# Performance work log

Hardware: AMD Instinct MI355X
Metric: run time of the kernel (lower is better)

## Reference

```python
import jax, jax.numpy as jnp
import numpy as np

B, N, FEAT, HID = 1024, 128, 512, 256


def setup_inputs() -> dict:
    key = jax.random.key(0)
    k1, k2, k3, k4, k5, k6 = jax.random.split(key, 6)
    x = jax.random.normal(k1, (B, FEAT), dtype=jnp.float32)
    labels = jax.random.randint(k2, (B,), 0, N, dtype=jnp.int64)
    W_proj = jax.random.normal(k3, (FEAT, HID), dtype=jnp.float32) / np.sqrt(FEAT)
    b_proj = jax.random.normal(k4, (HID,), dtype=jnp.float32) * 0.01
    means = jax.random.normal(k5, (N, HID), dtype=jnp.float32)
    # inverse covariances must be SPD so sqrt(dist_sq) is real
    A = jax.random.normal(k6, (N, HID, HID), dtype=jnp.float32)
    inv_covs = jnp.einsum('nij,nkj->nik', A, A) / HID + 0.1 * jnp.eye(HID, dtype=jnp.float32)
    return {"x": x, "labels": labels, "W_proj": W_proj, "b_proj": b_proj,
            "means": means, "inv_covs": inv_covs}


def reference(x, labels, W_proj, b_proj, means, inv_covs):
    b = x.shape[0]
    n = means.shape[0]
    x_proj = x @ W_proj + b_proj                       # (b, hid)
    delta = x_proj[:, None, :] - means[None, :, :]     # (b, n, hid)
    # batched Mahalanobis quadratic form
    dist_sq = jnp.einsum('bni,nij,bnj->bn', delta, inv_covs, delta)
    distmat = jnp.sqrt(dist_sq + 1e-12)                # (b, n)
    center_mask = (labels[:, None] == jnp.arange(n)[None, :]).astype(distmat.dtype)
    loss = jnp.clip(distmat * center_mask, 1e-12, 1e12).sum() / b
    return loss, distmat
```

## Files before the change

### kernel.cpp

```cpp
#include <hip/hip_runtime.h>
#include <hip/hip_bf16.h>

#define B_    1024
#define N_    128
#define FEAT_ 512
#define HID_  256

typedef __bf16 bf16x8 __attribute__((ext_vector_type(8)));
typedef float  f32x4  __attribute__((ext_vector_type(4)));

__device__ __forceinline__ unsigned int f2bf(float f) {
    unsigned int u = __float_as_uint(f);
    u += 0x7fffu + ((u >> 16) & 1u);
    return u >> 16;
}
__device__ __forceinline__ unsigned int pack2(float a, float b) {
    return f2bf(a) | (f2bf(b) << 16);
}

__global__ __launch_bounds__(256) void prep_kernel(
    const float* __restrict__ x, const float* __restrict__ W,
    const float* __restrict__ bias, const float* __restrict__ means,
    const float* __restrict__ invcov,
    float* __restrict__ xp, unsigned short* __restrict__ xbf,
    unsigned short* __restrict__ Mbf, float* __restrict__ v2,
    float* __restrict__ cpart)
{
    const int t = threadIdx.x;
    if (blockIdx.x < 512) {
        __shared__ float sv[64][33];
        const int n  = blockIdx.x >> 2;
        const int jq = blockIdx.x & 3;
        const float* Mn = invcov + (size_t)n * (HID_ * HID_) + (size_t)jq * 64 * HID_;
        const float* mu = means + (size_t)n * HID_;
        unsigned short* Mb = Mbf + (size_t)n * (HID_ * HID_) + (size_t)jq * 64 * HID_;
        const int gc = t & 31;
        const int r0 = t >> 5;
        const float4 mk0 = *(const float4*)(mu + gc * 8);
        const float4 mk1 = *(const float4*)(mu + gc * 8 + 4);
        #pragma unroll
        for (int i = 0; i < 8; ++i) {
            const int row = r0 + i * 8;
            const float* src = Mn + (size_t)row * HID_ + gc * 8;
            const float4 a = *(const float4*)src;
            const float4 b = *(const float4*)(src + 4);
            const int g2 = gc ^ ((row & 7) << 2);
            *(uint4*)(Mb + (size_t)row * HID_ + g2 * 8) =
                make_uint4(pack2(a.x, a.y), pack2(a.z, a.w), pack2(b.x, b.y), pack2(b.z, b.w));
            sv[row][gc] = a.x * mk0.x + a.y * mk0.y + a.z * mk0.z + a.w * mk0.w
                        + b.x * mk1.x + b.y * mk1.y + b.z * mk1.z + b.w * mk1.w;
        }
        __syncthreads();
        if (t < 64) {
            float v = 0.f;
            #pragma unroll
            for (int g = 0; g < 32; ++g) v += sv[t][g];
            const int j = jq * 64 + t;
            v2[(size_t)n * HID_ + j] = 2.f * v;
            float cc = v * mu[j];
            cc += __shfl_xor(cc, 1);
            cc += __shfl_xor(cc, 2);
            cc += __shfl_xor(cc, 4);
            cc += __shfl_xor(cc, 8);
            cc += __shfl_xor(cc, 16);
            cc += __shfl_xor(cc, 32);
            if (t == 0) cpart[n * 4 + jq] = cc;
        }
    } else {
        const int b0 = (blockIdx.x - 512) * 4;
        const int h  = t;
        const float bb = bias[h];
        float a0 = bb, a1 = bb, a2 = bb, a3 = bb;
        const float* x0p = x + (size_t)(b0 + 0) * FEAT_;
        const float* x1p = x + (size_t)(b0 + 1) * FEAT_;
        const float* x2p = x + (size_t)(b0 + 2) * FEAT_;
        const float* x3p = x + (size_t)(b0 + 3) * FEAT_;
        #pragma unroll 2
        for (int f = 0; f < FEAT_; f += 4) {
            const float4 xv0 = *(const float4*)(x0p + f);
            const float4 xv1 = *(const float4*)(x1p + f);
            const float4 xv2 = *(const float4*)(x2p + f);
            const float4 xv3 = *(const float4*)(x3p + f);
            const float w0 = W[(size_t)(f + 0) * HID_ + h];
            const float w1 = W[(size_t)(f + 1) * HID_ + h];
            const float w2 = W[(size_t)(f + 2) * HID_ + h];
            const float w3 = W[(size_t)(f + 3) * HID_ + h];
            a0 += xv0.x * w0 + xv0.y * w1 + xv0.z * w2 + xv0.w * w3;
            a1 += xv1.x * w0 + xv1.y * w1 + xv1.z * w2 + xv1.w * w3;
            a2 += xv2.x * w0 + xv2.y * w1 + xv2.z * w2 + xv2.w * w3;
            a3 += xv3.x * w0 + xv3.y * w1 + xv3.z * w2 + xv3.w * w3;
        }
        xp [(size_t)(b0 + 0) * HID_ + h] = a0;
        xp [(size_t)(b0 + 1) * HID_ + h] = a1;
        xp [(size_t)(b0 + 2) * HID_ + h] = a2;
        xp [(size_t)(b0 + 3) * HID_ + h] = a3;
        xbf[(size_t)(b0 + 0) * HID_ + h] = (unsigned short)f2bf(a0);
        xbf[(size_t)(b0 + 1) * HID_ + h] = (unsigned short)f2bf(a1);
        xbf[(size_t)(b0 + 2) * HID_ + h] = (unsigned short)f2bf(a2);
        xbf[(size_t)(b0 + 3) * HID_ + h] = (unsigned short)f2bf(a3);
    }
}

__global__ __launch_bounds__(512, 4) void dist_kernel(
    const float* __restrict__ xp, const unsigned short* __restrict__ xbf,
    const unsigned short* __restrict__ Mbf, const float* __restrict__ v2,
    float* __restrict__ p)
{
    extern __shared__ unsigned short Ms[];

    const int tid  = threadIdx.x;
    const int bh   = blockIdx.x;
    const int jh   = blockIdx.y;
    const int n    = blockIdx.z;
    const int wave = tid >> 6;
    const int lane = tid & 63;
    const int q    = lane >> 4;
    const int l    = lane & 15;

    const unsigned short* src = Mbf + (size_t)n * (HID_ * HID_) + (size_t)jh * 32768;
    #pragma unroll
    for (int i = 0; i < 8; ++i) {
        const int c = i * 8 + wave;
        __builtin_amdgcn_global_load_lds(
            (const __attribute__((address_space(1))) unsigned int*)(src + (size_t)c * 512 + lane * 8),
            (__attribute__((address_space(3))) unsigned int*)&Ms[c * 512],
            16, 0, 0);
    }

    bf16x8 afrag[2][8];
    #pragma unroll
    for (int rb = 0; rb < 2; ++rb) {
        const unsigned short* xr = xbf + (size_t)(bh * 256 + wave * 32 + rb * 16 + l) * HID_;
        #pragma unroll
        for (int kk = 0; kk < 8; ++kk)
            afrag[rb][kk] = *(const bf16x8*)(xr + kk * 32 + q * 8);
    }
    float v2l[8];
    #pragma unroll
    for (int ct = 0; ct < 8; ++ct)
        v2l[ct] = v2[(size_t)n * HID_ + jh * 128 + ct * 16 + l];

    __syncthreads();

    float part[8];
    #pragma unroll
    for (int i = 0; i < 8; ++i) part[i] = 0.f;

    const size_t xbase = (size_t)(bh * 256 + wave * 32 + q * 4) * HID_ + jh * 128 + l;

    #pragma unroll
    for (int ct = 0; ct < 8; ++ct) {
        float xl[8];
        #pragma unroll
        for (int rb = 0; rb < 2; ++rb)
            #pragma unroll
            for (int r = 0; r < 4; ++r)
                xl[rb * 4 + r] = xp[xbase + (size_t)(rb * 16 + r) * HID_ + ct * 16];

        f32x4 acc0 = {0.f,0.f,0.f,0.f}, acc1 = {0.f,0.f,0.f,0.f};
        #pragma unroll
        for (int kk = 0; kk < 8; ++kk) {
            const bf16x8 bfrag = *(const bf16x8*)&Ms[(ct * 16 + l) * HID_ +
                                                     (((kk * 4 + q) ^ ((l & 7) << 2)) << 3)];
            acc0 = __builtin_amdgcn_mfma_f32_16x16x32_bf16(afrag[0][kk], bfrag, acc0, 0, 0, 0);
            acc1 = __builtin_amdgcn_mfma_f32_16x16x32_bf16(afrag[1][kk], bfrag, acc1, 0, 0, 0);
        }
        const float vv = v2l[ct];
        #pragma unroll
        for (int r = 0; r < 4; ++r) {
            part[r]     += (acc0[r] - vv) * xl[r];
            part[4 + r] += (acc1[r] - vv) * xl[4 + r];
        }
    }

    #pragma unroll
    for (int i = 0; i < 8; ++i) {
        float v = part[i];
        v += __shfl_xor(v, 1);
        v += __shfl_xor(v, 2);
        v += __shfl_xor(v, 4);
        v += __shfl_xor(v, 8);
        part[i] = v;
    }
    if (l == 0) {
        float* pb = p + (size_t)jh * (B_ * N_);
        #pragma unroll
        for (int i = 0; i < 8; ++i) {
            const int row = bh * 256 + wave * 32 + (i >> 2) * 16 + q * 4 + (i & 3);
            pb[(size_t)row * N_ + n] = part[i];
        }
    }
}

__global__ __launch_bounds__(256) void finalize_kernel(
    const float* __restrict__ p, const float* __restrict__ cpart,
    float* __restrict__ out)
{
    const int i = blockIdx.x * 256 + threadIdx.x;
    const int n = i & (N_ - 1);
    const float c = cpart[n * 4] + cpart[n * 4 + 1] + cpart[n * 4 + 2] + cpart[n * 4 + 3];
    out[1 + i] = sqrtf(p[i] + p[B_ * N_ + i] + c + 1e-12f);
}

__global__ __launch_bounds__(1024) void loss_kernel(
    const float* __restrict__ distmat, const int* __restrict__ labels,
    float* __restrict__ out)
{
    __shared__ float red[16];
    const int b = threadIdx.x;
    float s = distmat[(size_t)b * N_ + labels[b]];
    #pragma unroll
    for (int m = 1; m <= 32; m <<= 1) s += __shfl_xor(s, m);
    if ((b & 63) == 0) red[b >> 6] = s;
    __syncthreads();
    if (b == 0) {
        float t = 0.f;
        #pragma unroll
        for (int i = 0; i < 16; ++i) t += red[i];
        out[0] = t / (float)B_ + (float)(N_ - 1) * 1e-12f;
    }
}

extern "C" void kernel_launch(void* const* d_in, const int* in_sizes, int n_in,
                              void* d_out, int out_size, void* d_ws, size_t ws_size,
                              hipStream_t stream) {
    const float* x      = (const float*)d_in[0];
    const int*   labels = (const int*)d_in[1];
    const float* W      = (const float*)d_in[2];
    const float* bias   = (const float*)d_in[3];
    const float* means  = (const float*)d_in[4];
    const float* invcov = (const float*)d_in[5];
    float* out = (float*)d_out;

    char* ws = (char*)d_ws;
    unsigned short* Mbf   = (unsigned short*)(ws);
    float*          xp    = (float*)         (ws + 16777216);
    unsigned short* xbf   = (unsigned short*)(ws + 17825792);
    float*          v2    = (float*)         (ws + 18350080);
    float*          cpart = (float*)         (ws + 18481152);
    float*          p     = (float*)         (ws + 18483200);

    constexpr int DIST_LDS = 128 * HID_ * 2;
    (void)hipFuncSetAttribute((const void*)dist_kernel,
                              hipFuncAttributeMaxDynamicSharedMemorySize, DIST_LDS);

    prep_kernel<<<dim3(768), 256, 0, stream>>>(x, W, bias, means, invcov,
                                               xp, xbf, Mbf, v2, cpart);
    dist_kernel<<<dim3(4, 2, N_), 512, DIST_LDS, stream>>>(xp, xbf, Mbf, v2, p);
    finalize_kernel<<<dim3((B_ * N_) / 256), 256, 0, stream>>>(p, cpart, out);
    loss_kernel<<<1, 1024, 0, stream>>>(out + 1, labels, out);
}
```

Baseline: 147.9 us.

## Split covariance prep into finer blocks and stage x rows in LDS for projection

The prep kernel now splits covariance conversion into 2048 blocks of 16 rows each instead of 512 blocks of 64 rows, which raises parallelism for the bandwidth-bound fp32 to bf16 pass over the 32 MB invcov. Projection blocks are placed first and load their four x rows into shared memory, so the inner loop reads x through LDS broadcasts instead of repeated global float4 loads. The cpart partials grow to 16 per class, so finalize now has every block sum 16 partials into shared memory. The cost is more blocks with short lifetimes and more redundant reduction work in finalize.

```diff
diff --git a/kernel.cpp b/kernel.cpp
--- a/kernel.cpp
+++ b/kernel.cpp
@@ -27,19 +27,51 @@
     float* __restrict__ cpart)
 {
     const int t = threadIdx.x;
-    if (blockIdx.x < 512) {
-        __shared__ float sv[64][33];
-        const int n  = blockIdx.x >> 2;
-        const int jq = blockIdx.x & 3;
-        const float* Mn = invcov + (size_t)n * (HID_ * HID_) + (size_t)jq * 64 * HID_;
+    if (blockIdx.x < 256) {
+        __shared__ float xs[4][FEAT_];
+        const int b0 = blockIdx.x * 4;
+        {
+            const float4* xsrc = (const float4*)(x + (size_t)b0 * FEAT_);
+            const float4 v0 = xsrc[t];
+            const float4 v1 = xsrc[t + 256];
+            ((float4*)&xs[0][0])[t]       = v0;
+            ((float4*)&xs[0][0])[t + 256] = v1;
+        }
+        __syncthreads();
+        const int h = t;
+        const float bb = bias[h];
+        float a0 = bb, a1 = bb, a2 = bb, a3 = bb;
+        #pragma unroll 8
+        for (int f = 0; f < FEAT_; ++f) {
+            const float w = W[(size_t)f * HID_ + h];
+            a0 += xs[0][f] * w;
+            a1 += xs[1][f] * w;
+            a2 += xs[2][f] * w;
+            a3 += xs[3][f] * w;
+        }
+        xp [(size_t)(b0 + 0) * HID_ + h] = a0;
+        xp [(size_t)(b0 + 1) * HID_ + h] = a1;
+        xp [(size_t)(b0 + 2) * HID_ + h] = a2;
+        xp [(size_t)(b0 + 3) * HID_ + h] = a3;
+        xbf[(size_t)(b0 + 0) * HID_ + h] = (unsigned short)f2bf(a0);
+        xbf[(size_t)(b0 + 1) * HID_ + h] = (unsigned short)f2bf(a1);
+        xbf[(size_t)(b0 + 2) * HID_ + h] = (unsigned short)f2bf(a2);
+        xbf[(size_t)(b0 + 3) * HID_ + h] = (unsigned short)f2bf(a3);
+    } else {
+        __shared__ float sv[16][33];
+        __shared__ float sw[2];
+        const int cb = blockIdx.x - 256;
+        const int n  = cb >> 4;
+        const int jg = cb & 15;
+        const float* Mn = invcov + (size_t)n * (HID_ * HID_) + (size_t)jg * 16 * HID_;
         const float* mu = means + (size_t)n * HID_;
-        unsigned short* Mb = Mbf + (size_t)n * (HID_ * HID_) + (size_t)jq * 64 * HID_;
+        unsigned short* Mb = Mbf + (size_t)n * (HID_ * HID_) + (size_t)jg * 16 * HID_;
         const int gc = t & 31;
         const int r0 = t >> 5;
         const float4 mk0 = *(const float4*)(mu + gc * 8);
         const float4 mk1 = *(const float4*)(mu + gc * 8 + 4);
         #pragma unroll
-        for (int i = 0; i < 8; ++i) {
+        for (int i = 0; i < 2; ++i) {
             const int row = r0 + i * 8;
             const float* src = Mn + (size_t)row * HID_ + gc * 8;
             const float4 a = *(const float4*)src;
@@ -51,53 +83,23 @@
                         + b.x * mk1.x + b.y * mk1.y + b.z * mk1.z + b.w * mk1.w;
         }
         __syncthreads();
-        if (t < 64) {
-            float v = 0.f;
-            #pragma unroll
-            for (int g = 0; g < 32; ++g) v += sv[t][g];
-            const int j = jq * 64 + t;
-            v2[(size_t)n * HID_ + j] = 2.f * v;
-            float cc = v * mu[j];
-            cc += __shfl_xor(cc, 1);
-            cc += __shfl_xor(cc, 2);
-            cc += __shfl_xor(cc, 4);
+        if (t < 128) {
+            const int row = t >> 3;
+            const int i0  = (t & 7) * 4;
+            float v = sv[row][i0] + sv[row][i0 + 1] + sv[row][i0 + 2] + sv[row][i0 + 3];
+            v += __shfl_xor(v, 1);
+            v += __shfl_xor(v, 2);
+            v += __shfl_xor(v, 4);
+            const int j = jg * 16 + row;
+            if ((t & 7) == 0) v2[(size_t)n * HID_ + j] = 2.f * v;
+            float cc = ((t & 7) == 0) ? v * mu[j] : 0.f;
             cc += __shfl_xor(cc, 8);
             cc += __shfl_xor(cc, 16);
             cc += __shfl_xor(cc, 32);
-            if (t == 0) cpart[n * 4 + jq] = cc;
-        }
-    } else {
-        const int b0 = (blockIdx.x - 512) * 4;
-        const int h  = t;
-        const float bb = bias[h];
-        float a0 = bb, a1 = bb, a2 = bb, a3 = bb;
-        const float* x0p = x + (size_t)(b0 + 0) * FEAT_;
-        const float* x1p = x + (size_t)(b0 + 1) * FEAT_;
-        const float* x2p = x + (size_t)(b0 + 2) * FEAT_;
-        const float* x3p = x + (size_t)(b0 + 3) * FEAT_;
-        #pragma unroll 2
-        for (int f = 0; f < FEAT_; f += 4) {
-            const float4 xv0 = *(const float4*)(x0p + f);
-            const float4 xv1 = *(const float4*)(x1p + f);
-            const float4 xv2 = *(const float4*)(x2p + f);
-            const float4 xv3 = *(const float4*)(x3p + f);
-            const float w0 = W[(size_t)(f + 0) * HID_ + h];
-            const float w1 = W[(size_t)(f + 1) * HID_ + h];
-            const float w2 = W[(size_t)(f + 2) * HID_ + h];
-            const float w3 = W[(size_t)(f + 3) * HID_ + h];
-            a0 += xv0.x * w0 + xv0.y * w1 + xv0.z * w2 + xv0.w * w3;
-            a1 += xv1.x * w0 + xv1.y * w1 + xv1.z * w2 + xv1.w * w3;
-            a2 += xv2.x * w0 + xv2.y * w1 + xv2.z * w2 + xv2.w * w3;
-            a3 += xv3.x * w0 + xv3.y * w1 + xv3.z * w2 + xv3.w * w3;
-        }
-        xp [(size_t)(b0 + 0) * HID_ + h] = a0;
-        xp [(size_t)(b0 + 1) * HID_ + h] = a1;
-        xp [(size_t)(b0 + 2) * HID_ + h] = a2;
-        xp [(size_t)(b0 + 3) * HID_ + h] = a3;
-        xbf[(size_t)(b0 + 0) * HID_ + h] = (unsigned short)f2bf(a0);
-        xbf[(size_t)(b0 + 1) * HID_ + h] = (unsigned short)f2bf(a1);
-        xbf[(size_t)(b0 + 2) * HID_ + h] = (unsigned short)f2bf(a2);
-        xbf[(size_t)(b0 + 3) * HID_ + h] = (unsigned short)f2bf(a3);
+            if ((t & 63) == 0) sw[t >> 6] = cc;
+        }
+        __syncthreads();
+        if (t == 0) cpart[cb] = sw[0] + sw[1];
     }
 }
 
@@ -196,10 +198,18 @@
     const float* __restrict__ p, const float* __restrict__ cpart,
     float* __restrict__ out)
 {
-    const int i = blockIdx.x * 256 + threadIdx.x;
+    __shared__ float sc[128];
+    const int t = threadIdx.x;
+    if (t < 128) {
+        float s = 0.f;
+        #pragma unroll
+        for (int g = 0; g < 16; ++g) s += cpart[t * 16 + g];
+        sc[t] = s;
+    }
+    __syncthreads();
+    const int i = blockIdx.x * 256 + t;
     const int n = i & (N_ - 1);
-    const float c = cpart[n * 4] + cpart[n * 4 + 1] + cpart[n * 4 + 2] + cpart[n * 4 + 3];
-    out[1 + i] = sqrtf(p[i] + p[B_ * N_ + i] + c + 1e-12f);
+    out[1 + i] = sqrtf(p[i] + p[B_ * N_ + i] + sc[n] + 1e-12f);
 }
 
 __global__ __launch_bounds__(1024) void loss_kernel(
@@ -238,14 +248,14 @@
     unsigned short* xbf   = (unsigned short*)(ws + 17825792);
     float*          v2    = (float*)         (ws + 18350080);
     float*          cpart = (float*)         (ws + 18481152);
-    float*          p     = (float*)         (ws + 18483200);
+    float*          p     = (float*)         (ws + 18489344);
 
     constexpr int DIST_LDS = 128 * HID_ * 2;
     (void)hipFuncSetAttribute((const void*)dist_kernel,
                               hipFuncAttributeMaxDynamicSharedMemorySize, DIST_LDS);
 
-    prep_kernel<<<dim3(768), 256, 0, stream>>>(x, W, bias, means, invcov,
-                                               xp, xbf, Mbf, v2, cpart);
+    prep_kernel<<<dim3(2304), 256, 0, stream>>>(x, W, bias, means, invcov,
+                                                xp, xbf, Mbf, v2, cpart);
     dist_kernel<<<dim3(4, 2, N_), 512, DIST_LDS, stream>>>(xp, xbf, Mbf, v2, p);
     finalize_kernel<<<dim3((B_ * N_) / 256), 256, 0, stream>>>(p, cpart, out);
     loss_kernel<<<1, 1024, 0, stream>>>(out + 1, labels, out);
```

New measurement: 146.5 us. No clear change (-0.9%).
